# Kernel tuning notes

Hardware: AMD Instinct MI355X
Metric: run time of the kernel (lower is better)

The kernel has to match this reference:

```python
import jax, jax.numpy as jnp
import numpy as np

B, S, D, H, DFF, NB = 32, 512, 256, 8, 1024, 2
L = NB + 2 * NB  # 2 blocks_1 + 4 blocks_2 = 6 layers, params stacked on axis 0
DK = D // H
NEG = jnp.float32(-1e32)


def _ln(x, s, b):
    mu = jnp.mean(x, -1, keepdims=True)
    var = jnp.mean((x - mu) ** 2, -1, keepdims=True)
    return (x - mu) * jax.lax.rsqrt(var + 1e-5) * s + b


def _attn(q, k, v, gamma, mask, zero_pad):
    # q,k,v: [B,H,S,DK]; mask: [1,1,S,S] bool; gamma: [H,1,1]
    scores = jnp.einsum('bhid,bhjd->bhij', q, k) / jnp.float32(np.sqrt(DK))
    # distance-decay effect (computed with no grad in the original)
    sc = jax.nn.softmax(jnp.where(mask, scores, NEG), axis=-1) * mask
    cum = jnp.cumsum(sc, axis=-1)
    tot = jnp.sum(sc, axis=-1, keepdims=True)
    idx = jnp.arange(S, dtype=jnp.float32)
    pos = jnp.abs(idx[None, :] - idx[:, None])[None, None]  # |i-j|
    dist = jax.lax.stop_gradient(jnp.sqrt(jnp.maximum((tot - cum) * pos, 0.0)))
    g = -jax.nn.softplus(gamma)[None]  # [1,H,1,1]
    eff = jnp.clip(jnp.exp(dist * g), 1e-5, 1e5)
    scores = jnp.where(mask, scores * eff, NEG)
    a = jax.nn.softmax(scores, axis=-1)
    if zero_pad:
        a = a.at[:, :, 0, :].set(0.0)
    return jnp.einsum('bhij,bhjd->bhid', a, v)


def _layer(i, mask_flag, q, k, v, apply_pos,
           Wk, bk, Wv, bv, Wo, bo, gammas, ln1_s, ln1_b, W1, b1, W2, b2, ln2_s, ln2_b):
    diag = 0 if mask_flag == 1 else -1  # mask=1: incl. diag; mask=0: strictly past
    mask = jnp.tril(jnp.ones((S, S), bool), diag)[None, None]
    to_h = lambda x, W, bb: (x @ W + bb).reshape(B, S, H, DK).transpose(0, 2, 1, 3)
    qh = to_h(q, Wk[i], bk[i])  # kq_same=True -> q uses k_linear
    kh = to_h(k, Wk[i], bk[i])
    vh = to_h(v, Wv[i], bv[i])
    o = _attn(qh, kh, vh, gammas[i], mask, zero_pad=(mask_flag == 0))
    o = o.transpose(0, 2, 1, 3).reshape(B, S, D) @ Wo[i] + bo[i]
    q = _ln(q + o, ln1_s[i], ln1_b[i])
    if apply_pos:
        f = jax.nn.relu(q @ W1[i] + b1[i]) @ W2[i] + b2[i]
        q = _ln(q + f, ln2_s[i], ln2_b[i])
    return q


def _forward(q_embed_data, qa_embed_data, *p):
    y, x = qa_embed_data, q_embed_data
    for i in range(NB):
        y = _layer(i, 1, y, y, y, True, *p)
    flag = True
    for j in range(2 * NB):
        i = NB + j
        if flag:
            x = _layer(i, 1, x, x, x, False, *p)
        else:
            x = _layer(i, 0, x, x, y, True, *p)
        flag = not flag
    return x


def setup_inputs() -> dict:
    key = jax.random.key(0)
    ks = jax.random.split(key, 9)
    sd = jnp.float32(1.0 / np.sqrt(D))
    sdf = jnp.float32(1.0 / np.sqrt(DFF))
    xb = float(np.sqrt(3.0))  # xavier bound for gammas (fan_in=fan_out=1)
    return {
        'q_embed_data': jax.random.normal(ks[0], (B, S, D), jnp.float32),
        'qa_embed_data': jax.random.normal(ks[1], (B, S, D), jnp.float32),
        'Wk': jax.random.normal(ks[2], (L, D, D), jnp.float32) * sd,
        'bk': jnp.zeros((L, D), jnp.float32),
        'Wv': jax.random.normal(ks[3], (L, D, D), jnp.float32) * sd,
        'bv': jnp.zeros((L, D), jnp.float32),
        'Wo': jax.random.normal(ks[4], (L, D, D), jnp.float32) * sd,
        'bo': jnp.zeros((L, D), jnp.float32),
        'gammas': jax.random.uniform(ks[5], (L, H, 1, 1), jnp.float32, -xb, xb),
        'ln1_s': jnp.ones((L, D), jnp.float32),
        'ln1_b': jnp.zeros((L, D), jnp.float32),
        'W1': jax.random.normal(ks[6], (L, D, DFF), jnp.float32) * sd,
        'b1': jnp.zeros((L, DFF), jnp.float32),
        'W2': jax.random.normal(ks[7], (L, DFF, D), jnp.float32) * sdf,
        'b2': jnp.zeros((L, D), jnp.float32),
        'ln2_s': jnp.ones((L, D), jnp.float32),
        'ln2_b': jnp.zeros((L, D), jnp.float32),
    }


def reference(q_embed_data, qa_embed_data, Wk, bk, Wv, bv, Wo, bo, gammas,
              ln1_s, ln1_b, W1, b1, W2, b2, ln2_s, ln2_b):
    return _forward(q_embed_data, qa_embed_data, Wk, bk, Wv, bv, Wo, bo, gammas,
                    ln1_s, ln1_b, W1, b1, W2, b2, ln2_s, ln2_b)
```

## Files before the change

### kernel.cpp

```cpp
#include <hip/hip_runtime.h>
#include <cstdint>
#include <cstddef>


#define AS1 __attribute__((address_space(1)))
#define AS3 __attribute__((address_space(3)))

typedef __bf16 bf16;
typedef __bf16 bf16x8 __attribute__((ext_vector_type(8)));
typedef __bf16 bf16x4 __attribute__((ext_vector_type(4)));
typedef __bf16 bf16x2 __attribute__((ext_vector_type(2)));
typedef float  f32x4  __attribute__((ext_vector_type(4)));
typedef float  f32x16 __attribute__((ext_vector_type(16)));
typedef unsigned int u32;

static constexpr int Mc = 32 * 512;

__global__ void cvt_copy2_kernel(const float* __restrict__ s0, float* __restrict__ da32,
                                 bf16* __restrict__ da16, const float* __restrict__ s1,
                                 float* __restrict__ db32, bf16* __restrict__ db16, int n4) {
  const float* s = blockIdx.y ? s1 : s0;
  float* d32 = blockIdx.y ? db32 : da32;
  bf16* d16 = blockIdx.y ? db16 : da16;
  int i = blockIdx.x * blockDim.x + threadIdx.x;
  if (i < n4) {
    float4 v = ((const float4*)s)[i];
    ((float4*)d32)[i] = v;
    bf16x4 hx = {(bf16)v.x, (bf16)v.y, (bf16)v.z, (bf16)v.w};
    ((bf16x4*)d16)[i] = hx;
  }
}

__global__ __launch_bounds__(256) void transpose_cvt_all(
    const float* __restrict__ Wk, const float* __restrict__ Wv, const float* __restrict__ Wo,
    const float* __restrict__ W1, const float* __restrict__ W2,
    bf16* __restrict__ Wkt, bf16* __restrict__ Wvt, bf16* __restrict__ Wot,
    bf16* __restrict__ W1t, bf16* __restrict__ W2t) {
  int z = blockIdx.z;
  int layer = z % 6, w = z / 6;
  const float* src; bf16* dst; int K, N;
  switch (w) {
    case 0: src = Wk; dst = Wkt; K = 256; N = 256; break;
    case 1: src = Wv; dst = Wvt; K = 256; N = 256; break;
    case 2: src = Wo; dst = Wot; K = 256; N = 256; break;
    case 3: src = W1; dst = W1t; K = 256; N = 1024; break;
    default: src = W2; dst = W2t; K = 1024; N = 256; break;
  }
  int k0 = blockIdx.x * 64, n0 = blockIdx.y * 64;
  if (k0 >= K || n0 >= N) return;
  src += (size_t)layer * K * N;
  dst += (size_t)layer * K * N;
  __shared__ bf16 t[64][68];
  int tid = threadIdx.x;
  int rr = tid >> 4;
  int c4 = (tid & 15) * 4;
#pragma unroll
  for (int p = 0; p < 4; ++p) {
    int k = rr + p * 16;
    float4 v = *(const float4*)(src + (size_t)(k0 + k) * N + n0 + c4);
    t[c4 + 0][k] = (bf16)v.x;
    t[c4 + 1][k] = (bf16)v.y;
    t[c4 + 2][k] = (bf16)v.z;
    t[c4 + 3][k] = (bf16)v.w;
  }
  __syncthreads();
#pragma unroll
  for (int p = 0; p < 4; ++p) {
    int nl = rr + p * 16;
    bf16x4 o4 = *(const bf16x4*)&t[nl][c4];
    *(bf16x4*)(dst + (size_t)(n0 + nl) * K + k0 + c4) = o4;
  }
}

template <int RELU, typename OUT_T>
__device__ __forceinline__ void gemm_body(
    const bf16* __restrict__ A, const bf16* __restrict__ Bt,
    const float* __restrict__ bias, OUT_T* __restrict__ C,
    int K, int N, int m0, int n0, bf16* As, bf16* Bs) {
  const int tid = threadIdx.x;
  const int lane = tid & 63;
  const int wid = tid >> 6;
  const int wm = (wid >> 1) * 64;
  const int wn = (wid & 1) * 64;
  f32x4 acc[4][4] = {};

  const int o1 = wid * 1024 + lane * 16;
  const int o2 = o1 + 4096;
  const int r1 = o1 >> 6, c1 = o1 & 63;
  const int r2 = o2 >> 6, c2 = o2 & 63;
  const char* Ab = (const char*)A;
  const char* Bb = (const char*)Bt;
  const size_t stride = (size_t)K * 2;

  auto stage_panel = [&](int panel, int kk) {
    const char* a1 = Ab + (size_t)(m0 + r1) * stride + (size_t)kk * 2 + c1;
    const char* a2 = Ab + (size_t)(m0 + r2) * stride + (size_t)kk * 2 + c2;
    const char* b1 = Bb + (size_t)(n0 + r1) * stride + (size_t)kk * 2 + c1;
    const char* b2 = Bb + (size_t)(n0 + r2) * stride + (size_t)kk * 2 + c2;
    char* ad = (char*)As + panel * 8192 + wid * 1024;
    char* bd = (char*)Bs + panel * 8192 + wid * 1024;
    __builtin_amdgcn_global_load_lds((const AS1 u32*)a1, (AS3 u32*)ad, 16, 0, 0);
    __builtin_amdgcn_global_load_lds((const AS1 u32*)a2, (AS3 u32*)(ad + 4096), 16, 0, 0);
    __builtin_amdgcn_global_load_lds((const AS1 u32*)b1, (AS3 u32*)bd, 16, 0, 0);
    __builtin_amdgcn_global_load_lds((const AS1 u32*)b2, (AS3 u32*)(bd + 4096), 16, 0, 0);
  };

  stage_panel(0, 0);
  stage_panel(1, 32);
  asm volatile("s_waitcnt vmcnt(0)" ::: "memory");
  __syncthreads();

  int cur = 0;
  for (int k0 = 0; k0 < K; k0 += 64) {
    if (k0 + 64 < K) {
      stage_panel((cur ^ 1) * 2, k0 + 64);
      stage_panel((cur ^ 1) * 2 + 1, k0 + 96);
    }
    const int rr = lane & 15;
    const int g8 = (lane >> 4) * 8;
#pragma unroll
    for (int s = 0; s < 2; ++s) {
      const int base = (cur * 2 + s) * 4096;
      bf16x8 af[4], bfr[4];
#pragma unroll
      for (int i = 0; i < 4; ++i) {
        af[i]  = *(const bf16x8*)&As[base + (wm + i * 16 + rr) * 32 + g8];
        bfr[i] = *(const bf16x8*)&Bs[base + (wn + i * 16 + rr) * 32 + g8];
      }
#pragma unroll
      for (int mi = 0; mi < 4; ++mi)
#pragma unroll
        for (int ni = 0; ni < 4; ++ni)
          acc[mi][ni] = __builtin_amdgcn_mfma_f32_16x16x32_bf16(af[mi], bfr[ni], acc[mi][ni], 0, 0, 0);
    }
    asm volatile("s_waitcnt vmcnt(0)" ::: "memory");
    __syncthreads();
    cur ^= 1;
  }

  const int rr = lane & 15;
  const int g4 = (lane >> 4) * 4;
  float bv[4];
#pragma unroll
  for (int ni = 0; ni < 4; ++ni) bv[ni] = bias[n0 + wn + ni * 16 + rr];
#pragma unroll
  for (int mi = 0; mi < 4; ++mi)
#pragma unroll
    for (int ni = 0; ni < 4; ++ni)
#pragma unroll
      for (int r = 0; r < 4; ++r) {
        float v = acc[mi][ni][r] + bv[ni];
        if (RELU) v = fmaxf(v, 0.f);
        int row = m0 + wm + mi * 16 + g4 + r;
        int col = n0 + wn + ni * 16 + rr;
        C[(size_t)row * N + col] = (OUT_T)v;
      }
}

template <int RELU, typename OUT_T>
__global__ __launch_bounds__(256) void gemm_bias_kernel(
    const bf16* __restrict__ A, const bf16* __restrict__ Bt,
    const float* __restrict__ bias, OUT_T* __restrict__ C, int K, int N) {
  __shared__ bf16 As[4 * 4096];
  __shared__ bf16 Bs[4 * 4096];
  gemm_body<RELU, OUT_T>(A, Bt, bias, C, K, N, blockIdx.x * 128, blockIdx.y * 128, As, Bs);
}

__global__ __launch_bounds__(256) void gemm_kv_kernel(
    const bf16* __restrict__ A0, const bf16* __restrict__ Bt0,
    const float* __restrict__ b0, bf16* __restrict__ C0,
    const bf16* __restrict__ A1, const bf16* __restrict__ Bt1,
    const float* __restrict__ b1, bf16* __restrict__ C1, int K, int N) {
  __shared__ bf16 As[4 * 4096];
  __shared__ bf16 Bs[4 * 4096];
  int sel = blockIdx.y >> 1;
  gemm_body<0, bf16>(sel ? A1 : A0, sel ? Bt1 : Bt0, sel ? b1 : b0, sel ? C1 : C0,
                     K, N, blockIdx.x * 128, (blockIdx.y & 1) * 128, As, Bs);
}

template <int KSZ>
__global__ __launch_bounds__(512, 4) void gemm_ln_kernel(
    const bf16* __restrict__ A, const bf16* __restrict__ Bt,
    const float* __restrict__ bias, const float* __restrict__ resid,
    const float* __restrict__ lns, const float* __restrict__ lnb,
    float* __restrict__ out32, bf16* __restrict__ out16) {
  __shared__ bf16 As[2 * 32 * 32];
  __shared__ bf16 Bs[2 * 256 * 32];
  __shared__ float wsum[8][16][2];
  __shared__ float stats[32][2];
  const int tid = threadIdx.x, lane = tid & 63, wid = tid >> 6;
  const int m0 = blockIdx.x * 32;
  const int wr = wid >> 2, wc = wid & 3;
  f32x4 acc[4] = {};
  const char* Ab = (const char*)A;
  const char* Bb = (const char*)Bt;
  const size_t stride = (size_t)KSZ * 2;

  auto stage = [&](int buf, int kk) {
    if (wid < 2) {
      int off = wid * 1024 + lane * 16;
      const char* a1 = Ab + (size_t)(m0 + (off >> 6)) * stride + (size_t)kk * 2 + (off & 63);
      __builtin_amdgcn_global_load_lds((const AS1 u32*)a1,
                                       (AS3 u32*)((char*)As + buf * 2048 + wid * 1024), 16, 0, 0);
    }
    int off1 = wid * 2048 + lane * 16;
    int off2 = off1 + 1024;
    const char* b1 = Bb + (size_t)(off1 >> 6) * stride + (size_t)kk * 2 + (off1 & 63);
    const char* b2 = Bb + (size_t)(off2 >> 6) * stride + (size_t)kk * 2 + (off2 & 63);
    char* bd = (char*)Bs + buf * 16384 + wid * 2048;
    __builtin_amdgcn_global_load_lds((const AS1 u32*)b1, (AS3 u32*)bd, 16, 0, 0);
    __builtin_amdgcn_global_load_lds((const AS1 u32*)b2, (AS3 u32*)(bd + 1024), 16, 0, 0);
  };

  stage(0, 0);
  asm volatile("s_waitcnt vmcnt(0)" ::: "memory");
  __syncthreads();

  int cur = 0;
  for (int k0 = 0; k0 < KSZ; k0 += 32) {
    if (k0 + 32 < KSZ) stage(cur ^ 1, k0 + 32);
    const int rr = lane & 15, g8 = (lane >> 4) * 8;
    bf16x8 af = *(const bf16x8*)&As[cur * 1024 + (wr * 16 + rr) * 32 + g8];
    bf16x8 bfr[4];
#pragma unroll
    for (int ni = 0; ni < 4; ++ni)
      bfr[ni] = *(const bf16x8*)&Bs[cur * 8192 + (wc * 64 + ni * 16 + rr) * 32 + g8];
#pragma unroll
    for (int ni = 0; ni < 4; ++ni)
      acc[ni] = __builtin_amdgcn_mfma_f32_16x16x32_bf16(af, bfr[ni], acc[ni], 0, 0, 0);
    asm volatile("s_waitcnt vmcnt(0)" ::: "memory");
    __syncthreads();
    cur ^= 1;
  }

  const int rr = lane & 15, g4 = (lane >> 4) * 4;
  float bv[4], scv[4], biv[4];
  int col[4];
#pragma unroll
  for (int ni = 0; ni < 4; ++ni) {
    col[ni] = wc * 64 + ni * 16 + rr;
    bv[ni] = bias[col[ni]];
    scv[ni] = lns[col[ni]];
    biv[ni] = lnb[col[ni]];
  }
  float v[4][4];
#pragma unroll
  for (int r = 0; r < 4; ++r) {
    int grow = m0 + wr * 16 + g4 + r;
#pragma unroll
    for (int ni = 0; ni < 4; ++ni)
      v[ni][r] = acc[ni][r] + bv[ni] + resid[(size_t)grow * 256 + col[ni]];
  }
#pragma unroll
  for (int r = 0; r < 4; ++r) {
    float s1 = (v[0][r] + v[1][r]) + (v[2][r] + v[3][r]);
    float s2 = (v[0][r] * v[0][r] + v[1][r] * v[1][r]) + (v[2][r] * v[2][r] + v[3][r] * v[3][r]);
#pragma unroll
    for (int off = 8; off; off >>= 1) {
      s1 += __shfl_xor(s1, off);
      s2 += __shfl_xor(s2, off);
    }
    if (rr == 0) {
      int lrow = wr * 16 + g4 + r;
      wsum[wid][lrow & 15][0] = s1;
      wsum[wid][lrow & 15][1] = s2;
    }
  }
  __syncthreads();
  if (tid < 32) {
    int row = tid;
    int band = row >> 4;
    float s1 = 0.f, s2 = 0.f;
#pragma unroll
    for (int k = 0; k < 4; ++k) {
      s1 += wsum[band * 4 + k][row & 15][0];
      s2 += wsum[band * 4 + k][row & 15][1];
    }
    float mu = s1 * (1.f / 256.f);
    float var = s2 * (1.f / 256.f) - mu * mu;
    stats[row][0] = mu;
    stats[row][1] = rsqrtf(var + 1e-5f);
  }
  __syncthreads();
#pragma unroll
  for (int r = 0; r < 4; ++r) {
    int lrow = wr * 16 + g4 + r;
    int grow = m0 + lrow;
    float mu = stats[lrow][0], rs = stats[lrow][1];
#pragma unroll
    for (int ni = 0; ni < 4; ++ni) {
      float y = (v[ni][r] - mu) * rs * scv[ni] + biv[ni];
      out32[(size_t)grow * 256 + col[ni]] = y;
      out16[(size_t)grow * 256 + col[ni]] = (bf16)y;
    }
  }
}

__global__ __launch_bounds__(512, 4) void gemm_ln_ffn1_kernel(
    const bf16* __restrict__ A, const bf16* __restrict__ Bt,
    const float* __restrict__ bias, const float* __restrict__ resid,
    const float* __restrict__ lns, const float* __restrict__ lnb,
    float* __restrict__ out32, bf16* __restrict__ out16,
    const bf16* __restrict__ W1t, const float* __restrict__ b1,
    bf16* __restrict__ h116) {
  __shared__ bf16 As[2 * 32 * 32];
  __shared__ bf16 Bs[2 * 256 * 32];
  __shared__ bf16 vL[32 * 264];
  __shared__ float wsum[8][16][2];
  __shared__ float stats[32][2];
  const int tid = threadIdx.x, lane = tid & 63, wid = tid >> 6;
  const int m0 = blockIdx.x * 32;
  const int wr = wid >> 2, wc = wid & 3;
  f32x4 acc[4] = {};
  const char* Ab = (const char*)A;
  const char* Bb = (const char*)Bt;
  const size_t stride = (size_t)256 * 2;

  auto stage = [&](int buf, int kk) {
    if (wid < 2) {
      int off = wid * 1024 + lane * 16;
      const char* a1 = Ab + (size_t)(m0 + (off >> 6)) * stride + (size_t)kk * 2 + (off & 63);
      __builtin_amdgcn_global_load_lds((const AS1 u32*)a1,
                                       (AS3 u32*)((char*)As + buf * 2048 + wid * 1024), 16, 0, 0);
    }
    int off1 = wid * 2048 + lane * 16;
    int off2 = off1 + 1024;
    const char* b1p = Bb + (size_t)(off1 >> 6) * stride + (size_t)kk * 2 + (off1 & 63);
    const char* b2p = Bb + (size_t)(off2 >> 6) * stride + (size_t)kk * 2 + (off2 & 63);
    char* bd = (char*)Bs + buf * 16384 + wid * 2048;
    __builtin_amdgcn_global_load_lds((const AS1 u32*)b1p, (AS3 u32*)bd, 16, 0, 0);
    __builtin_amdgcn_global_load_lds((const AS1 u32*)b2p, (AS3 u32*)(bd + 1024), 16, 0, 0);
  };

  stage(0, 0);
  asm volatile("s_waitcnt vmcnt(0)" ::: "memory");
  __syncthreads();

  int cur = 0;
  for (int k0 = 0; k0 < 256; k0 += 32) {
    if (k0 + 32 < 256) stage(cur ^ 1, k0 + 32);
    const int rr = lane & 15, g8 = (lane >> 4) * 8;
    bf16x8 af = *(const bf16x8*)&As[cur * 1024 + (wr * 16 + rr) * 32 + g8];
    bf16x8 bfr[4];
#pragma unroll
    for (int ni = 0; ni < 4; ++ni)
      bfr[ni] = *(const bf16x8*)&Bs[cur * 8192 + (wc * 64 + ni * 16 + rr) * 32 + g8];
#pragma unroll
    for (int ni = 0; ni < 4; ++ni)
      acc[ni] = __builtin_amdgcn_mfma_f32_16x16x32_bf16(af, bfr[ni], acc[ni], 0, 0, 0);
    asm volatile("s_waitcnt vmcnt(0)" ::: "memory");
    __syncthreads();
    cur ^= 1;
  }

  {
    const int rr = lane & 15, g4 = (lane >> 4) * 4;
    float bv[4], scv[4], biv[4];
    int col[4];
#pragma unroll
    for (int ni = 0; ni < 4; ++ni) {
      col[ni] = wc * 64 + ni * 16 + rr;
      bv[ni] = bias[col[ni]];
      scv[ni] = lns[col[ni]];
      biv[ni] = lnb[col[ni]];
    }
    float v[4][4];
#pragma unroll
    for (int r = 0; r < 4; ++r) {
      int grow = m0 + wr * 16 + g4 + r;
#pragma unroll
      for (int ni = 0; ni < 4; ++ni)
        v[ni][r] = acc[ni][r] + bv[ni] + resid[(size_t)grow * 256 + col[ni]];
    }
#pragma unroll
    for (int r = 0; r < 4; ++r) {
      float s1 = (v[0][r] + v[1][r]) + (v[2][r] + v[3][r]);
      float s2 = (v[0][r] * v[0][r] + v[1][r] * v[1][r]) + (v[2][r] * v[2][r] + v[3][r] * v[3][r]);
#pragma unroll
      for (int off = 8; off; off >>= 1) {
        s1 += __shfl_xor(s1, off);
        s2 += __shfl_xor(s2, off);
      }
      if (rr == 0) {
        int lrow = wr * 16 + g4 + r;
        wsum[wid][lrow & 15][0] = s1;
        wsum[wid][lrow & 15][1] = s2;
      }
    }
    __syncthreads();
    if (tid < 32) {
      int row = tid;
      int band = row >> 4;
      float s1 = 0.f, s2 = 0.f;
#pragma unroll
      for (int k = 0; k < 4; ++k) {
        s1 += wsum[band * 4 + k][row & 15][0];
        s2 += wsum[band * 4 + k][row & 15][1];
      }
      float mu = s1 * (1.f / 256.f);
      float var = s2 * (1.f / 256.f) - mu * mu;
      stats[row][0] = mu;
      stats[row][1] = rsqrtf(var + 1e-5f);
    }
    __syncthreads();
#pragma unroll
    for (int r = 0; r < 4; ++r) {
      int lrow = wr * 16 + g4 + r;
      int grow = m0 + lrow;
      float mu = stats[lrow][0], rs = stats[lrow][1];
#pragma unroll
      for (int ni = 0; ni < 4; ++ni) {
        float y = (v[ni][r] - mu) * rs * scv[ni] + biv[ni];
        out32[(size_t)grow * 256 + col[ni]] = y;
        out16[(size_t)grow * 256 + col[ni]] = (bf16)y;
        vL[lrow * 264 + col[ni]] = (bf16)y;
      }
    }
  }

  const char* W1b = (const char*)W1t;
  auto stage2 = [&](int buf, int nb, int kk) {
    int off1 = wid * 2048 + lane * 16;
    int off2 = off1 + 1024;
    const char* b1p = W1b + (size_t)(nb * 256 + (off1 >> 6)) * stride + (size_t)kk * 2 + (off1 & 63);
    const char* b2p = W1b + (size_t)(nb * 256 + (off2 >> 6)) * stride + (size_t)kk * 2 + (off2 & 63);
    char* bd = (char*)Bs + buf * 16384 + wid * 2048;
    __builtin_amdgcn_global_load_lds((const AS1 u32*)b1p, (AS3 u32*)bd, 16, 0, 0);
    __builtin_amdgcn_global_load_lds((const AS1 u32*)b2p, (AS3 u32*)(bd + 1024), 16, 0, 0);
  };

  for (int nb = 0; nb < 4; ++nb) {
    stage2(0, nb, 0);
    asm volatile("s_waitcnt vmcnt(0)" ::: "memory");
    __syncthreads();
    f32x4 acc2[4] = {};
    int c2 = 0;
    for (int k0 = 0; k0 < 256; k0 += 32) {
      if (k0 + 32 < 256) stage2(c2 ^ 1, nb, k0 + 32);
      const int rr = lane & 15, g8 = (lane >> 4) * 8;
      bf16x8 af = *(const bf16x8*)&vL[(wr * 16 + rr) * 264 + k0 + g8];
      bf16x8 bfr[4];
#pragma unroll
      for (int ni = 0; ni < 4; ++ni)
        bfr[ni] = *(const bf16x8*)&Bs[c2 * 8192 + (wc * 64 + ni * 16 + rr) * 32 + g8];
#pragma unroll
      for (int ni = 0; ni < 4; ++ni)
        acc2[ni] = __builtin_amdgcn_mfma_f32_16x16x32_bf16(af, bfr[ni], acc2[ni], 0, 0, 0);
      asm volatile("s_waitcnt vmcnt(0)" ::: "memory");
      __syncthreads();
      c2 ^= 1;
    }
    const int rr = lane & 15, g4 = (lane >> 4) * 4;
#pragma unroll
    for (int ni = 0; ni < 4; ++ni) {
      int colh = nb * 256 + wc * 64 + ni * 16 + rr;
      float bb = b1[colh];
#pragma unroll
      for (int r = 0; r < 4; ++r) {
        int grow = m0 + wr * 16 + g4 + r;
        float hv = fmaxf(acc2[ni][r] + bb, 0.f);
        h116[(size_t)grow * 1024 + colh] = (bf16)hv;
      }
    }
  }
}

static constexpr int LDK = 34;
static constexpr int LDV = 534;
static constexpr float LOG2E = 1.4426950408889634f;
static constexpr float KSC = 0.17677669529663687f * LOG2E;

__device__ __forceinline__ int jloc(int r, int hi) { return (r & 3) + 8 * (r >> 2) + 4 * hi; }

__device__ __forceinline__ u32 pkbf(float x, float y) {
  bf16x2 t = {(bf16)x, (bf16)y};
  return __builtin_bit_cast(u32, t);
}

__device__ __forceinline__ void plswap(u32& a, u32& b) {
  asm volatile("v_permlane32_swap_b32 %0, %1" : "+v"(a), "+v"(b));
}

__device__ __forceinline__ f32x16 qk_tile(const bf16* Klds, int jbase, int lq,
                                          const bf16x8& qf0, const bf16x8& qf1, int hi) {
  const bf16x8 ka0 = *(const bf16x8*)&Klds[(jbase + lq) * LDK + hi * 8];
  const bf16x8 ka1 = *(const bf16x8*)&Klds[(jbase + lq) * LDK + 16 + hi * 8];
  f32x16 c = {};
  c = __builtin_amdgcn_mfma_f32_32x32x16_bf16(ka0, qf0, c, 0, 0, 0);
  c = __builtin_amdgcn_mfma_f32_32x32x16_bf16(ka1, qf1, c, 0, 0, 0);
  return c;
}

template <bool MASKED>
__device__ __forceinline__ void tileA(const f32x16& c, int jbase, int hi, int qlim, float& tot) {
  float t[4] = {0.f, 0.f, 0.f, 0.f};
#pragma unroll
  for (int q2 = 0; q2 < 4; ++q2)
#pragma unroll
    for (int p = 0; p < 4; ++p) {
      const int r = q2 * 4 + p;
      float e = __builtin_amdgcn_exp2f(c[r] * KSC);
      if (MASKED) {
        int j = jbase + 8 * q2 + 4 * hi + p;
        if (j > qlim) e = 0.f;
      }
      t[q2] += e;
    }
  tot += (t[0] + t[1]) + (t[2] + t[3]);
}

template <bool MASKED>
__device__ __forceinline__ void tileB(const f32x16& c, int jbase, int lq, int hi,
                                      int qlim, float itot, float gneg2, float posf,
                                      const bf16* Vt, float& run, float& sum2, f32x16& pvacc) {
  float su2[16], lcs[16], G[4];
#pragma unroll
  for (int q2 = 0; q2 < 4; ++q2) {
    float a = 0.f;
#pragma unroll
    for (int p = 0; p < 4; ++p) {
      const int r = q2 * 4 + p;
      su2[r] = c[r] * KSC;
      float e = __builtin_amdgcn_exp2f(su2[r]);
      if (MASKED) {
        int j = jbase + 8 * q2 + 4 * hi + p;
        if (j > qlim) e = 0.f;
      }
      a += e;
      lcs[r] = a;
    }
    G[q2] = a;
  }
  float Po[4];
#pragma unroll
  for (int q2 = 0; q2 < 4; ++q2) Po[q2] = __shfl_xor(G[q2], 32);
  float base[4];
  {
    float pre = run;
#pragma unroll
    for (int q2 = 0; q2 < 4; ++q2) {
      base[q2] = pre + (hi ? Po[q2] : 0.f);
      pre += G[q2] + Po[q2];
    }
    run = pre;
  }
#pragma unroll
  for (int cc = 0; cc < 2; ++cc) {
    float pv[8];
#pragma unroll
    for (int q2s = 0; q2s < 2; ++q2s) {
      const int q2 = cc * 2 + q2s;
#pragma unroll
      for (int p = 0; p < 4; ++p) {
        const int r = q2 * 4 + p;
        float cum = base[q2] + lcs[r];
        float pos = posf - (float)(8 * q2 + p);
        float d2 = fmaxf(__builtin_fmaf(-cum, itot, 1.f) * pos, 0.f);
        float dist = __builtin_amdgcn_sqrtf(d2);
        float eff = fmaxf(__builtin_amdgcn_exp2f(dist * gneg2), 1e-5f);
        float t = __builtin_amdgcn_exp2f(su2[r] * eff);
        if (MASKED) {
          int j = jbase + 8 * q2 + 4 * hi + p;
          if (j > qlim) t = 0.f;
        }
        pv[q2s * 4 + p] = t;
      }
    }
    sum2 += ((pv[0] + pv[1]) + (pv[2] + pv[3])) + ((pv[4] + pv[5]) + (pv[6] + pv[7]));
    u32 a0 = pkbf(pv[0], pv[1]);
    u32 a1 = pkbf(pv[2], pv[3]);
    u32 b0 = pkbf(pv[4], pv[5]);
    u32 b1 = pkbf(pv[6], pv[7]);
    plswap(a0, b0);
    plswap(a1, b1);
    uint4 fq; fq.x = a0; fq.y = a1; fq.z = b0; fq.w = b1;
    bf16x8 pa = __builtin_bit_cast(bf16x8, fq);
    bf16x8 vb = *(const bf16x8*)&Vt[(size_t)lq * LDV + jbase + cc * 16 + hi * 8];
    pvacc = __builtin_amdgcn_mfma_f32_32x32x16_bf16(pa, vb, pvacc, 0, 0, 0);
  }
}

__global__ __launch_bounds__(1024, 4) void attn_kernel(
    const bf16* __restrict__ kh, const bf16* __restrict__ vh,
    const float* __restrict__ gam, bf16* __restrict__ o, int incl_diag) {
  __shared__ bf16 Klds[512 * LDK];
  __shared__ bf16 Vt[32 * LDV];
  __shared__ float exA[8][32];
  __shared__ float exB[8][32];
  __shared__ float s2A[8][32];
  __shared__ float pvp[8][32][32];

  const int tid = threadIdx.x;
  const int lane = tid & 63;
  const int wid = tid >> 6;
  const int bh = blockIdx.x;
  const int b = bh >> 3, h = bh & 7;
  const bf16* kbase = kh + ((size_t)b * 4096 + h) * 32;
  const bf16* vbase = vh + ((size_t)b * 4096 + h) * 32;
  bf16* obase = o + ((size_t)b * 4096 + h) * 32;

#pragma unroll
  for (int it = 0; it < 2; ++it) {
    int t = it * 1024 + tid;
    int j = t >> 2, cc = t & 3;
    bf16x8 kv8 = *(const bf16x8*)(kbase + (size_t)j * 256 + cc * 8);
    *(bf16x8*)&Klds[j * LDK + cc * 8] = kv8;
  }
  {
    int u = tid & 255;
    int cg = tid >> 8;
    const bf16* vb = vbase + (size_t)(2 * u) * 256 + cg * 8;
    bf16x8 r0 = *(const bf16x8*)(vb);
    bf16x8 r1 = *(const bf16x8*)(vb + 256);
#pragma unroll
    for (int e = 0; e < 8; ++e) {
      bf16x2 w2 = {r0[e], r1[e]};
      *(bf16x2*)&Vt[(size_t)(cg * 8 + e) * LDV + 2 * u] = w2;
    }
  }
  __syncthreads();

  float gm = gam[h];
  float gneg = -(fmaxf(gm, 0.f) + log1pf(__expf(-fabsf(gm))));
  const float gneg2 = gneg * LOG2E;
  const int lq = lane & 31;
  const int hi = lane >> 5;

  const int p = wid & 7;
  const bool front = wid < 8;
  const int f = 7 - p;
  const int qbHi = 15 - p;
  const int ntHi = 16 - p;
  const int q0Hi = qbHi * 32;
  const int qrHi = q0Hi + lq;
  const int qlimHi = incl_diag ? qrHi : qrHi - 1;
  const int q0Lo = p * 32;
  const int qrLo = q0Lo + lq;
  const int qlimLo = incl_diag ? qrLo : qrLo - 1;

  const bf16x8 qfH0 = *(const bf16x8*)&Klds[(q0Hi + lq) * LDK + hi * 8];
  const bf16x8 qfH1 = *(const bf16x8*)&Klds[(q0Hi + lq) * LDK + 16 + hi * 8];

  float totLo = 0.f, S = 0.f;
  if (front) {
    const bf16x8 qfL0 = *(const bf16x8*)&Klds[(q0Lo + lq) * LDK + hi * 8];
    const bf16x8 qfL1 = *(const bf16x8*)&Klds[(q0Lo + lq) * LDK + 16 + hi * 8];
    for (int jt = 0; jt < p; ++jt) {
      f32x16 c = qk_tile(Klds, jt * 32, lq, qfL0, qfL1, hi);
      tileA<false>(c, jt * 32, hi, qlimLo, totLo);
    }
    {
      f32x16 c = qk_tile(Klds, q0Lo, lq, qfL0, qfL1, hi);
      tileA<true>(c, q0Lo, hi, qlimLo, totLo);
    }
    totLo += __shfl_xor(totLo, 32);
    for (int jt = 0; jt < f; ++jt) {
      f32x16 c = qk_tile(Klds, jt * 32, lq, qfH0, qfH1, hi);
      tileA<false>(c, jt * 32, hi, qlimHi, S);
    }
    S += __shfl_xor(S, 32);
    if (lane < 32) exA[p][lq] = S;
  } else {
    for (int jt = f; jt < ntHi - 1; ++jt) {
      f32x16 c = qk_tile(Klds, jt * 32, lq, qfH0, qfH1, hi);
      tileA<false>(c, jt * 32, hi, qlimHi, S);
    }
    {
      f32x16 c = qk_tile(Klds, q0Hi, lq, qfH0, qfH1, hi);
      tileA<true>(c, q0Hi, hi, qlimHi, S);
    }
    S += __shfl_xor(S, 32);
    if (lane < 32) exB[p][lq] = S;
  }
  __syncthreads();
  const float SA = exA[p][lq];
  const float SB = exB[p][lq];
  const float totHi = SA + SB;
  const float itotHi = totHi > 0.f ? 1.f / totHi : 0.f;

  f32x16 pvHi = {};
  float sum2Hi = 0.f;
  if (front) {
    const bf16x8 qfL0 = *(const bf16x8*)&Klds[(q0Lo + lq) * LDK + hi * 8];
    const bf16x8 qfL1 = *(const bf16x8*)&Klds[(q0Lo + lq) * LDK + 16 + hi * 8];
    const float itotLo = totLo > 0.f ? 1.f / totLo : 0.f;
    f32x16 pvLo = {};
    float sum2Lo = 0.f, run = 0.f;
    float posf = (float)(qrLo - 4 * hi);
    for (int jt = 0; jt < p; ++jt) {
      f32x16 c = qk_tile(Klds, jt * 32, lq, qfL0, qfL1, hi);
      tileB<false>(c, jt * 32, lq, hi, qlimLo, itotLo, gneg2, posf, Vt, run, sum2Lo, pvLo);
      posf -= 32.f;
    }
    {
      f32x16 c = qk_tile(Klds, q0Lo, lq, qfL0, qfL1, hi);
      tileB<true>(c, q0Lo, lq, hi, qlimLo, itotLo, gneg2, posf, Vt, run, sum2Lo, pvLo);
    }
    sum2Lo += __shfl_xor(sum2Lo, 32);
    const float inv2Lo = sum2Lo > 0.f ? 1.f / sum2Lo : 0.f;
#pragma unroll
    for (int r = 0; r < 16; ++r) {
      int qv = jloc(r, hi);
      float iv = __shfl(inv2Lo, qv);
      obase[(size_t)(q0Lo + qv) * 256 + lq] = (bf16)(pvLo[r] * iv);
    }
    run = 0.f;
    posf = (float)(qrHi - 4 * hi);
    for (int jt = 0; jt < f; ++jt) {
      f32x16 c = qk_tile(Klds, jt * 32, lq, qfH0, qfH1, hi);
      tileB<false>(c, jt * 32, lq, hi, qlimHi, itotHi, gneg2, posf, Vt, run, sum2Hi, pvHi);
      posf -= 32.f;
    }
    sum2Hi += __shfl_xor(sum2Hi, 32);
    if (lane < 32) s2A[p][lq] = sum2Hi;
#pragma unroll
    for (int r = 0; r < 16; ++r) pvp[p][jloc(r, hi)][lq] = pvHi[r];
  } else {
    float run = SA;
    float posf = (float)(qrHi - 4 * hi - 32 * f);
    for (int jt = f; jt < ntHi - 1; ++jt) {
      f32x16 c = qk_tile(Klds, jt * 32, lq, qfH0, qfH1, hi);
      tileB<false>(c, jt * 32, lq, hi, qlimHi, itotHi, gneg2, posf, Vt, run, sum2Hi, pvHi);
      posf -= 32.f;
    }
    {
      f32x16 c = qk_tile(Klds, q0Hi, lq, qfH0, qfH1, hi);
      tileB<true>(c, q0Hi, lq, hi, qlimHi, itotHi, gneg2, posf, Vt, run, sum2Hi, pvHi);
    }
    sum2Hi += __shfl_xor(sum2Hi, 32);
  }
  __syncthreads();
  if (!front) {
    const float s2 = s2A[p][lq] + sum2Hi;
    const float inv2 = s2 > 0.f ? 1.f / s2 : 0.f;
#pragma unroll
    for (int r = 0; r < 16; ++r) {
      int qv = jloc(r, hi);
      float iv = __shfl(inv2, qv);
      float val = pvHi[r] + pvp[p][qv][lq];
      obase[(size_t)(q0Hi + qv) * 256 + lq] = (bf16)(val * iv);
    }
  }
}

extern "C" void kernel_launch(void* const* d_in, const int* in_sizes, int n_in,
                              void* d_out, int out_size, void* d_ws, size_t ws_size,
                              hipStream_t stream) {
  const float* q_embed  = (const float*)d_in[0];
  const float* qa_embed = (const float*)d_in[1];
  const float* Wk = (const float*)d_in[2];
  const float* bk = (const float*)d_in[3];
  const float* Wv = (const float*)d_in[4];
  const float* bv = (const float*)d_in[5];
  const float* Wo = (const float*)d_in[6];
  const float* bo = (const float*)d_in[7];
  const float* gammas = (const float*)d_in[8];
  const float* ln1_s = (const float*)d_in[9];
  const float* ln1_b = (const float*)d_in[10];
  const float* W1 = (const float*)d_in[11];
  const float* b1 = (const float*)d_in[12];
  const float* W2 = (const float*)d_in[13];
  const float* b2 = (const float*)d_in[14];
  const float* ln2_s = (const float*)d_in[15];
  const float* ln2_b = (const float*)d_in[16];
  float* out = (float*)d_out;

  char* ws = (char*)d_ws;
  float* y32 = (float*)(ws);
  float* x32 = (float*)(ws + ((size_t)16 << 20));
  bf16* y16  = (bf16*)(ws + ((size_t)32 << 20));
  bf16* x16  = (bf16*)(ws + ((size_t)40 << 20));
  bf16* khb  = (bf16*)(ws + ((size_t)48 << 20));
  bf16* vhb  = (bf16*)(ws + ((size_t)56 << 20));
  bf16* o16  = (bf16*)(ws + ((size_t)64 << 20));
  bf16* h116 = (bf16*)(ws + ((size_t)88 << 20));
  bf16* Wkt  = (bf16*)(ws + ((size_t)122 << 20));
  bf16* Wvt  = Wkt + 6 * 65536;
  bf16* Wot  = Wvt + 6 * 65536;
  bf16* W1t  = Wot + 6 * 65536;
  bf16* W2t  = W1t + 6 * 262144;

  transpose_cvt_all<<<dim3(16, 16, 30), 256, 0, stream>>>(Wk, Wv, Wo, W1, W2,
                                                          Wkt, Wvt, Wot, W1t, W2t);
  cvt_copy2_kernel<<<dim3(4096, 2), 256, 0, stream>>>(q_embed, x32, x16,
                                                      qa_embed, y32, y16, Mc * 256 / 4);

  for (int i = 0; i < 6; ++i) {
    const bool first = (i < 2);
    const bool strict = (i == 3 || i == 5);
    const bool pos = first || strict;
    bf16* in16 = first ? y16 : x16;
    bf16* v16  = (first || strict) ? y16 : x16;
    float* res32 = first ? y32 : x32;

    gemm_kv_kernel<<<dim3(128, 4), 256, 0, stream>>>(
        in16, Wkt + (size_t)i * 65536, bk + i * 256, khb,
        v16, Wvt + (size_t)i * 65536, bv + i * 256, vhb, 256, 256);
    attn_kernel<<<256, 1024, 0, stream>>>(khb, vhb, gammas + i * 8, o16, strict ? 0 : 1);
    if (pos) {
      gemm_ln_ffn1_kernel<<<512, 512, 0, stream>>>(
          o16, Wot + (size_t)i * 65536, bo + i * 256, res32,
          ln1_s + i * 256, ln1_b + i * 256, res32, in16,
          W1t + (size_t)i * 262144, b1 + i * 1024, h116);
      float* fin = (i == 5) ? out : res32;
      gemm_ln_kernel<1024><<<512, 512, 0, stream>>>(
          h116, W2t + (size_t)i * 262144, b2 + i * 256, res32,
          ln2_s + i * 256, ln2_b + i * 256, fin, in16);
    } else {
      gemm_ln_kernel<256><<<512, 512, 0, stream>>>(
          o16, Wot + (size_t)i * 65536, bo + i * 256, res32,
          ln1_s + i * 256, ln1_b + i * 256, res32, in16);
    }
  }
}
```

Before: 605.6 us.

## Fuse FFN second GEMM and LayerNorm into the Wo+LN+FFN1 kernel

Merges the Wo GEMM + LN1, FFN1 and FFN2 GEMM + LN2 into one kernel per 32-row block. Each 256-wide hidden chunk is computed into LDS (hch) and immediately consumed by a partial W2 GEMM accumulated in registers. This removes the 32 MB bf16 hidden-activation round trip through global memory, one kernel launch, and the fp32 residual reload. In exchange it adds LDS pressure, which may lower occupancy, and each block now runs its GEMMs serially with weights restaged per block.

```diff
diff --git a/kernel.cpp b/kernel.cpp
--- a/kernel.cpp
+++ b/kernel.cpp
@@ -155,15 +155,6 @@
         int col = n0 + wn + ni * 16 + rr;
         C[(size_t)row * N + col] = (OUT_T)v;
       }
-}
-
-template <int RELU, typename OUT_T>
-__global__ __launch_bounds__(256) void gemm_bias_kernel(
-    const bf16* __restrict__ A, const bf16* __restrict__ Bt,
-    const float* __restrict__ bias, OUT_T* __restrict__ C, int K, int N) {
-  __shared__ bf16 As[4 * 4096];
-  __shared__ bf16 Bs[4 * 4096];
-  gemm_body<RELU, OUT_T>(A, Bt, bias, C, K, N, blockIdx.x * 128, blockIdx.y * 128, As, Bs);
 }
 
 __global__ __launch_bounds__(256) void gemm_kv_kernel(
@@ -296,50 +287,57 @@
   }
 }
 
-__global__ __launch_bounds__(512, 4) void gemm_ln_ffn1_kernel(
+__global__ __launch_bounds__(512, 4) void gemm_ln_ffn_kernel(
     const bf16* __restrict__ A, const bf16* __restrict__ Bt,
     const float* __restrict__ bias, const float* __restrict__ resid,
     const float* __restrict__ lns, const float* __restrict__ lnb,
-    float* __restrict__ out32, bf16* __restrict__ out16,
     const bf16* __restrict__ W1t, const float* __restrict__ b1,
-    bf16* __restrict__ h116) {
+    const bf16* __restrict__ W2t, const float* __restrict__ b2,
+    const float* __restrict__ ln2s, const float* __restrict__ ln2b,
+    float* __restrict__ out32, bf16* __restrict__ out16) {
   __shared__ bf16 As[2 * 32 * 32];
   __shared__ bf16 Bs[2 * 256 * 32];
   __shared__ bf16 vL[32 * 264];
+  __shared__ bf16 hch[32 * 264];
   __shared__ float wsum[8][16][2];
   __shared__ float stats[32][2];
   const int tid = threadIdx.x, lane = tid & 63, wid = tid >> 6;
   const int m0 = blockIdx.x * 32;
   const int wr = wid >> 2, wc = wid & 3;
-  f32x4 acc[4] = {};
+  const int rr = lane & 15, g4 = (lane >> 4) * 4, g8 = (lane >> 4) * 8;
   const char* Ab = (const char*)A;
   const char* Bb = (const char*)Bt;
-  const size_t stride = (size_t)256 * 2;
-
-  auto stage = [&](int buf, int kk) {
+  const size_t strideA = 512;
+  const size_t strideW1 = 512;
+  const size_t strideW2 = 2048;
+
+  int col[4];
+#pragma unroll
+  for (int ni = 0; ni < 4; ++ni) col[ni] = wc * 64 + ni * 16 + rr;
+
+  auto stage1 = [&](int buf, int kk) {
     if (wid < 2) {
       int off = wid * 1024 + lane * 16;
-      const char* a1 = Ab + (size_t)(m0 + (off >> 6)) * stride + (size_t)kk * 2 + (off & 63);
+      const char* a1 = Ab + (size_t)(m0 + (off >> 6)) * strideA + (size_t)kk * 2 + (off & 63);
       __builtin_amdgcn_global_load_lds((const AS1 u32*)a1,
                                        (AS3 u32*)((char*)As + buf * 2048 + wid * 1024), 16, 0, 0);
     }
     int off1 = wid * 2048 + lane * 16;
     int off2 = off1 + 1024;
-    const char* b1p = Bb + (size_t)(off1 >> 6) * stride + (size_t)kk * 2 + (off1 & 63);
-    const char* b2p = Bb + (size_t)(off2 >> 6) * stride + (size_t)kk * 2 + (off2 & 63);
+    const char* b1p = Bb + (size_t)(off1 >> 6) * strideA + (size_t)kk * 2 + (off1 & 63);
+    const char* b2p = Bb + (size_t)(off2 >> 6) * strideA + (size_t)kk * 2 + (off2 & 63);
     char* bd = (char*)Bs + buf * 16384 + wid * 2048;
     __builtin_amdgcn_global_load_lds((const AS1 u32*)b1p, (AS3 u32*)bd, 16, 0, 0);
     __builtin_amdgcn_global_load_lds((const AS1 u32*)b2p, (AS3 u32*)(bd + 1024), 16, 0, 0);
   };
 
-  stage(0, 0);
+  f32x4 acc[4] = {};
+  stage1(0, 0);
   asm volatile("s_waitcnt vmcnt(0)" ::: "memory");
   __syncthreads();
-
   int cur = 0;
   for (int k0 = 0; k0 < 256; k0 += 32) {
-    if (k0 + 32 < 256) stage(cur ^ 1, k0 + 32);
-    const int rr = lane & 15, g8 = (lane >> 4) * 8;
+    if (k0 + 32 < 256) stage1(cur ^ 1, k0 + 32);
     bf16x8 af = *(const bf16x8*)&As[cur * 1024 + (wr * 16 + rr) * 32 + g8];
     bf16x8 bfr[4];
 #pragma unroll
@@ -353,13 +351,11 @@
     cur ^= 1;
   }
 
+  float y[4][4];
   {
-    const int rr = lane & 15, g4 = (lane >> 4) * 4;
     float bv[4], scv[4], biv[4];
-    int col[4];
 #pragma unroll
     for (int ni = 0; ni < 4; ++ni) {
-      col[ni] = wc * 64 + ni * 16 + rr;
       bv[ni] = bias[col[ni]];
       scv[ni] = lns[col[ni]];
       biv[ni] = lnb[col[ni]];
@@ -406,39 +402,78 @@
 #pragma unroll
     for (int r = 0; r < 4; ++r) {
       int lrow = wr * 16 + g4 + r;
-      int grow = m0 + lrow;
       float mu = stats[lrow][0], rs = stats[lrow][1];
 #pragma unroll
       for (int ni = 0; ni < 4; ++ni) {
-        float y = (v[ni][r] - mu) * rs * scv[ni] + biv[ni];
-        out32[(size_t)grow * 256 + col[ni]] = y;
-        out16[(size_t)grow * 256 + col[ni]] = (bf16)y;
-        vL[lrow * 264 + col[ni]] = (bf16)y;
-      }
-    }
-  }
+        float yy = (v[ni][r] - mu) * rs * scv[ni] + biv[ni];
+        y[ni][r] = yy;
+        vL[lrow * 264 + col[ni]] = (bf16)yy;
+      }
+    }
+  }
+  __syncthreads();
 
   const char* W1b = (const char*)W1t;
-  auto stage2 = [&](int buf, int nb, int kk) {
+  const char* W2b = (const char*)W2t;
+  f32x4 acc2[4] = {};
+
+  auto stageW1 = [&](int buf, int nb, int kk) {
     int off1 = wid * 2048 + lane * 16;
     int off2 = off1 + 1024;
-    const char* b1p = W1b + (size_t)(nb * 256 + (off1 >> 6)) * stride + (size_t)kk * 2 + (off1 & 63);
-    const char* b2p = W1b + (size_t)(nb * 256 + (off2 >> 6)) * stride + (size_t)kk * 2 + (off2 & 63);
+    const char* b1p = W1b + (size_t)(nb * 256 + (off1 >> 6)) * strideW1 + (size_t)kk * 2 + (off1 & 63);
+    const char* b2p = W1b + (size_t)(nb * 256 + (off2 >> 6)) * strideW1 + (size_t)kk * 2 + (off2 & 63);
     char* bd = (char*)Bs + buf * 16384 + wid * 2048;
     __builtin_amdgcn_global_load_lds((const AS1 u32*)b1p, (AS3 u32*)bd, 16, 0, 0);
     __builtin_amdgcn_global_load_lds((const AS1 u32*)b2p, (AS3 u32*)(bd + 1024), 16, 0, 0);
   };
+  auto stageW2 = [&](int buf, int nb, int kk) {
+    int off1 = wid * 2048 + lane * 16;
+    int off2 = off1 + 1024;
+    const char* b1p = W2b + (size_t)(off1 >> 6) * strideW2 + (size_t)(nb * 256 + kk) * 2 + (off1 & 63);
+    const char* b2p = W2b + (size_t)(off2 >> 6) * strideW2 + (size_t)(nb * 256 + kk) * 2 + (off2 & 63);
+    char* bd = (char*)Bs + buf * 16384 + wid * 2048;
+    __builtin_amdgcn_global_load_lds((const AS1 u32*)b1p, (AS3 u32*)bd, 16, 0, 0);
+    __builtin_amdgcn_global_load_lds((const AS1 u32*)b2p, (AS3 u32*)(bd + 1024), 16, 0, 0);
+  };
 
   for (int nb = 0; nb < 4; ++nb) {
-    stage2(0, nb, 0);
+    f32x4 acc1[4] = {};
+    stageW1(0, nb, 0);
     asm volatile("s_waitcnt vmcnt(0)" ::: "memory");
     __syncthreads();
-    f32x4 acc2[4] = {};
+    int c1 = 0;
+    for (int k0 = 0; k0 < 256; k0 += 32) {
+      if (k0 + 32 < 256) stageW1(c1 ^ 1, nb, k0 + 32);
+      bf16x8 af = *(const bf16x8*)&vL[(wr * 16 + rr) * 264 + k0 + g8];
+      bf16x8 bfr[4];
+#pragma unroll
+      for (int ni = 0; ni < 4; ++ni)
+        bfr[ni] = *(const bf16x8*)&Bs[c1 * 8192 + (wc * 64 + ni * 16 + rr) * 32 + g8];
+#pragma unroll
+      for (int ni = 0; ni < 4; ++ni)
+        acc1[ni] = __builtin_amdgcn_mfma_f32_16x16x32_bf16(af, bfr[ni], acc1[ni], 0, 0, 0);
+      asm volatile("s_waitcnt vmcnt(0)" ::: "memory");
+      __syncthreads();
+      c1 ^= 1;
+    }
+#pragma unroll
+    for (int ni = 0; ni < 4; ++ni) {
+      float bb = b1[nb * 256 + col[ni]];
+#pragma unroll
+      for (int r = 0; r < 4; ++r) {
+        int lrow = wr * 16 + g4 + r;
+        hch[lrow * 264 + col[ni]] = (bf16)fmaxf(acc1[ni][r] + bb, 0.f);
+      }
+    }
+    __syncthreads();
+
+    stageW2(0, nb, 0);
+    asm volatile("s_waitcnt vmcnt(0)" ::: "memory");
+    __syncthreads();
     int c2 = 0;
     for (int k0 = 0; k0 < 256; k0 += 32) {
-      if (k0 + 32 < 256) stage2(c2 ^ 1, nb, k0 + 32);
-      const int rr = lane & 15, g8 = (lane >> 4) * 8;
-      bf16x8 af = *(const bf16x8*)&vL[(wr * 16 + rr) * 264 + k0 + g8];
+      if (k0 + 32 < 256) stageW2(c2 ^ 1, nb, k0 + 32);
+      bf16x8 af = *(const bf16x8*)&hch[(wr * 16 + rr) * 264 + k0 + g8];
       bf16x8 bfr[4];
 #pragma unroll
       for (int ni = 0; ni < 4; ++ni)
@@ -450,16 +485,63 @@
       __syncthreads();
       c2 ^= 1;
     }
-    const int rr = lane & 15, g4 = (lane >> 4) * 4;
+  }
+
+  {
+    float bv[4], scv[4], biv[4];
 #pragma unroll
     for (int ni = 0; ni < 4; ++ni) {
-      int colh = nb * 256 + wc * 64 + ni * 16 + rr;
-      float bb = b1[colh];
-#pragma unroll
-      for (int r = 0; r < 4; ++r) {
-        int grow = m0 + wr * 16 + g4 + r;
-        float hv = fmaxf(acc2[ni][r] + bb, 0.f);
-        h116[(size_t)grow * 1024 + colh] = (bf16)hv;
+      bv[ni] = b2[col[ni]];
+      scv[ni] = ln2s[col[ni]];
+      biv[ni] = ln2b[col[ni]];
+    }
+    float v[4][4];
+#pragma unroll
+    for (int r = 0; r < 4; ++r)
+#pragma unroll
+      for (int ni = 0; ni < 4; ++ni)
+        v[ni][r] = y[ni][r] + acc2[ni][r] + bv[ni];
+#pragma unroll
+    for (int r = 0; r < 4; ++r) {
+      float s1 = (v[0][r] + v[1][r]) + (v[2][r] + v[3][r]);
+      float s2 = (v[0][r] * v[0][r] + v[1][r] * v[1][r]) + (v[2][r] * v[2][r] + v[3][r] * v[3][r]);
+#pragma unroll
+      for (int off = 8; off; off >>= 1) {
+        s1 += __shfl_xor(s1, off);
+        s2 += __shfl_xor(s2, off);
+      }
+      if (rr == 0) {
+        int lrow = wr * 16 + g4 + r;
+        wsum[wid][lrow & 15][0] = s1;
+        wsum[wid][lrow & 15][1] = s2;
+      }
+    }
+    __syncthreads();
+    if (tid < 32) {
+      int row = tid;
+      int band = row >> 4;
+      float s1 = 0.f, s2 = 0.f;
+#pragma unroll
+      for (int k = 0; k < 4; ++k) {
+        s1 += wsum[band * 4 + k][row & 15][0];
+        s2 += wsum[band * 4 + k][row & 15][1];
+      }
+      float mu = s1 * (1.f / 256.f);
+      float var = s2 * (1.f / 256.f) - mu * mu;
+      stats[row][0] = mu;
+      stats[row][1] = rsqrtf(var + 1e-5f);
+    }
+    __syncthreads();
+#pragma unroll
+    for (int r = 0; r < 4; ++r) {
+      int lrow = wr * 16 + g4 + r;
+      int grow = m0 + lrow;
+      float mu = stats[lrow][0], rs = stats[lrow][1];
+#pragma unroll
+      for (int ni = 0; ni < 4; ++ni) {
+        float yy = (v[ni][r] - mu) * rs * scv[ni] + biv[ni];
+        out32[(size_t)grow * 256 + col[ni]] = yy;
+        out16[(size_t)grow * 256 + col[ni]] = (bf16)yy;
       }
     }
   }
@@ -773,7 +855,6 @@
   bf16* khb  = (bf16*)(ws + ((size_t)48 << 20));
   bf16* vhb  = (bf16*)(ws + ((size_t)56 << 20));
   bf16* o16  = (bf16*)(ws + ((size_t)64 << 20));
-  bf16* h116 = (bf16*)(ws + ((size_t)88 << 20));
   bf16* Wkt  = (bf16*)(ws + ((size_t)122 << 20));
   bf16* Wvt  = Wkt + 6 * 65536;
   bf16* Wot  = Wvt + 6 * 65536;
@@ -798,13 +879,12 @@
         v16, Wvt + (size_t)i * 65536, bv + i * 256, vhb, 256, 256);
     attn_kernel<<<256, 1024, 0, stream>>>(khb, vhb, gammas + i * 8, o16, strict ? 0 : 1);
     if (pos) {
-      gemm_ln_ffn1_kernel<<<512, 512, 0, stream>>>(
+      float* fin = (i == 5) ? out : res32;
+      gemm_ln_ffn_kernel<<<512, 512, 0, stream>>>(
           o16, Wot + (size_t)i * 65536, bo + i * 256, res32,
-          ln1_s + i * 256, ln1_b + i * 256, res32, in16,
-          W1t + (size_t)i * 262144, b1 + i * 1024, h116);
-      float* fin = (i == 5) ? out : res32;
-      gemm_ln_kernel<1024><<<512, 512, 0, stream>>>(
-          h116, W2t + (size_t)i * 262144, b2 + i * 256, res32,
+          ln1_s + i * 256, ln1_b + i * 256,
+          W1t + (size_t)i * 262144, b1 + i * 1024,
+          W2t + (size_t)i * 262144, b2 + i * 256,
           ln2_s + i * 256, ln2_b + i * 256, fin, in16);
     } else {
       gemm_ln_kernel<256><<<512, 512, 0, stream>>>(
```

Measured after the change: 570.8 us. -5.7%, faster.
